# Kernel optimization log

Measured on AMD Instinct MI355X. Metric: run time of the kernel, lower is better.

Reference implementation:

```python
import jax, jax.numpy as jnp
import numpy as np

V = 50000      # vocab_size
E = 300        # EMBED_SIZE
H = 128        # HIDDEN_SIZE // NUM_DIRS
T = 12         # num_tags
SOS = 3
EOS = 4
NEG = -10000.0


def setup_inputs() -> dict:
    key = jax.random.key(0)
    ks = jax.random.split(key, 14)
    B, S = 128, 512
    x = jax.random.randint(ks[0], (B, S), 0, V)
    y0 = jax.random.randint(ks[1], (B, S), 0, T)
    s = 1.0 / np.sqrt(H)
    u = lambda k, shape: jax.random.uniform(k, shape, jnp.float32, -s, s)
    embed = jax.random.normal(ks[2], (V, E), jnp.float32)
    # torch LSTM gate layout: [i, f, g, o] stacked along first dim (4H)
    Wih_f = u(ks[3], (4 * H, E)); Whh_f = u(ks[4], (4 * H, H)); b_f = u(ks[5], (4 * H,)) + u(ks[6], (4 * H,))
    Wih_b = u(ks[7], (4 * H, E)); Whh_b = u(ks[8], (4 * H, H)); b_b = u(ks[9], (4 * H,)) + u(ks[10], (4 * H,))
    Wout = u(ks[11], (T, 2 * H)); bout = u(ks[12], (T,))
    trans = jax.random.normal(ks[13], (T, T), jnp.float32)
    trans = trans.at[SOS, :].set(NEG).at[:, EOS].set(NEG)
    return dict(x=x, y0=y0, embed=embed,
                Wih_f=Wih_f, Whh_f=Whh_f, b_f=b_f,
                Wih_b=Wih_b, Whh_b=Whh_b, b_b=b_b,
                Wout=Wout, bout=bout, trans=trans)


def _lstm_dir(emb, Wih, Whh, b):
    # emb: [B, S, E] -> hidden states [B, S, H] for one direction
    B = emb.shape[0]
    def step(carry, x_t):
        h, c = carry
        g = x_t @ Wih.T + h @ Whh.T + b  # [B, 4H]
        i, f, gg, o = jnp.split(g, 4, axis=-1)
        c = jax.nn.sigmoid(f) * c + jax.nn.sigmoid(i) * jnp.tanh(gg)
        h = jax.nn.sigmoid(o) * jnp.tanh(c)
        return (h, c), h
    init = (jnp.zeros((B, H), emb.dtype), jnp.zeros((B, H), emb.dtype))
    _, hs = jax.lax.scan(step, init, jnp.swapaxes(emb, 0, 1))  # hs: [S, B, H]
    return jnp.swapaxes(hs, 0, 1)


def reference(x, y0, embed, Wih_f, Whh_f, b_f, Wih_b, Whh_b, b_b, Wout, bout, trans):
    # ---- lstm: embed -> biLSTM -> linear, emissions y: [B, S, T]
    emb = embed[x]
    hf = _lstm_dir(emb, Wih_f, Whh_f, b_f)
    hb = _lstm_dir(emb[:, ::-1], Wih_b, Whh_b, b_b)[:, ::-1]
    y = jnp.concatenate([hf, hb], axis=-1) @ Wout.T + bout

    B = x.shape[0]
    # ---- CRF partition Z via forward algorithm (trans[i, j] = score j -> i)
    score0 = jnp.full((B, T), NEG, y.dtype).at[:, SOS].set(0.0)
    def step(score, emit_t):
        new = jax.nn.logsumexp(score[:, None, :] + trans[None, :, :], axis=-1) + emit_t
        return new, None
    scoreZ, _ = jax.lax.scan(step, score0, jnp.swapaxes(y, 0, 1))
    Z = jax.nn.logsumexp(scoreZ + trans[EOS][None, :], axis=-1)  # [B]

    # ---- gold path score (vectorized version of crf.score)
    y0p = jnp.concatenate([jnp.full((B, 1), SOS, y0.dtype), y0], axis=1)  # [B, S+1]
    emit = jnp.take_along_axis(y, y0p[:, 1:, None], axis=2)[..., 0].sum(axis=1)
    tr = trans[y0p[:, 1:], y0p[:, :-1]].sum(axis=1)
    gold = emit + tr + trans[EOS, y0p[:, -1]]

    return Z - gold  # [B] negative log-likelihood per example
```

## Files before the change

kernel.cpp:

```cpp
#include <hip/hip_runtime.h>

typedef unsigned short u16;
typedef __attribute__((ext_vector_type(8))) short short8;
typedef __attribute__((ext_vector_type(4))) float floatx4;

#define SOS 3
#define EOS 4
#define NEGV -10000.0f
#define LOG2E 1.442695041f
#define TWOLOG2E 2.885390082f

__device__ __forceinline__ u16 f2bf(float f) {
  union { float f; unsigned int i; } v; v.f = f;
  unsigned int r = (v.i + 0x7FFFu + ((v.i >> 16) & 1u)) >> 16;
  return (u16)r;
}
__device__ __forceinline__ void gload_lds16(const u16* g, u16* l) {
  __builtin_amdgcn_global_load_lds((const __attribute__((address_space(1))) void*)g,
                                   (__attribute__((address_space(3))) void*)l, 16, 0, 0);
}

__global__ __launch_bounds__(256) void gather_kernel(const float* __restrict__ embed,
                                                     const int* __restrict__ x,
                                                     u16* __restrict__ A) {
  int idx = blockIdx.x * 256 + threadIdx.x;
  int row = idx / 40;
  int c8 = idx - row * 40;
  int col0 = c8 * 8;
  int b = row & 127, t = row >> 7;
  const float* src = embed + (size_t)x[b * 512 + t] * 300 + col0;
  short8 o;
  if (col0 + 8 <= 300) {
    float4 f0 = *(const float4*)(src);
    float4 f1 = *(const float4*)(src + 4);
    o[0] = (short)f2bf(f0.x); o[1] = (short)f2bf(f0.y);
    o[2] = (short)f2bf(f0.z); o[3] = (short)f2bf(f0.w);
    o[4] = (short)f2bf(f1.x); o[5] = (short)f2bf(f1.y);
    o[6] = (short)f2bf(f1.z); o[7] = (short)f2bf(f1.w);
  } else {
    #pragma unroll
    for (int e = 0; e < 8; ++e)
      o[e] = (col0 + e < 300) ? (short)f2bf(src[e]) : (short)0;
  }
  *(short8*)&A[(size_t)row * 320 + col0] = o;
}

__global__ __launch_bounds__(256) void wpack_kernel(const float* __restrict__ Wf,
                                                    const float* __restrict__ Wb,
                                                    u16* __restrict__ Wp) {
  int idx = blockIdx.x * 256 + threadIdx.x;
  int p = idx / 40;
  int c8 = idx - p * 40;
  int col0 = c8 * 8;
  int dd = p >> 9, q = p & 511;
  int j = q >> 2, g = q & 3;
  const float* src = (dd ? Wb : Wf) + (size_t)(g * 128 + j) * 300;
  short8 o;
  #pragma unroll
  for (int e = 0; e < 8; ++e)
    o[e] = (col0 + e < 300) ? (short)f2bf(src[col0 + e]) : (short)0;
  *(short8*)&Wp[(size_t)p * 320 + col0] = o;
}

__global__ __launch_bounds__(256) void gemm_kernel(const u16* __restrict__ A,
                                                   const u16* __restrict__ B,
                                                   const float* __restrict__ bf_,
                                                   const float* __restrict__ bb_,
                                                   u16* __restrict__ G) {
  __shared__ u16 At[128 * 32];
  __shared__ u16 Bt[128 * 32];
  const int n = blockIdx.x;
  const int xcd = n & 7, rr = n >> 3;
  const int bx = xcd * 64 + (rr >> 3);
  const int by = rr & 7;
  const int tid = threadIdx.x;
  const int lane = tid & 63;
  const int wave = tid >> 6;
  const int wr = wave >> 1, wc = wave & 1;
  const int arow0 = bx * 128;
  const int bcol0 = by * 128;
  floatx4 acc[4][4] = {};
  const int fq = lane >> 4;
  const int fr = lane & 15;
  const int sr = wave * 32 + (lane >> 2);
  const int sc = (lane & 3) * 8;
  for (int k0 = 0; k0 < 320; k0 += 32) {
    #pragma unroll
    for (int q = 0; q < 2; ++q) {
      gload_lds16(&A[(size_t)(arow0 + sr + q * 16) * 320 + k0 + sc], &At[wave * 1024 + q * 512]);
      gload_lds16(&B[(size_t)(bcol0 + sr + q * 16) * 320 + k0 + sc], &Bt[wave * 1024 + q * 512]);
    }
    __syncthreads();
    short8 af[4], bfr[4];
    #pragma unroll
    for (int mi = 0; mi < 4; ++mi)
      af[mi] = *(const short8*)&At[(wr * 64 + mi * 16 + fr) * 32 + fq * 8];
    #pragma unroll
    for (int ni = 0; ni < 4; ++ni)
      bfr[ni] = *(const short8*)&Bt[(wc * 64 + ni * 16 + fr) * 32 + fq * 8];
    #pragma unroll
    for (int mi = 0; mi < 4; ++mi)
      #pragma unroll
      for (int ni = 0; ni < 4; ++ni)
        acc[mi][ni] = __builtin_amdgcn_mfma_f32_16x16x32_bf16(af[mi], bfr[ni], acc[mi][ni], 0, 0, 0);
    __syncthreads();
  }
  float biasv[4];
  #pragma unroll
  for (int ni = 0; ni < 4; ++ni) {
    int col = bcol0 + wc * 64 + ni * 16 + fr;
    int dd = col >> 9, q = col & 511;
    int jj = q >> 2, gg = q & 3;
    biasv[ni] = (dd ? bb_ : bf_)[gg * 128 + jj];
  }
  #pragma unroll
  for (int mi = 0; mi < 4; ++mi)
    #pragma unroll
    for (int ni = 0; ni < 4; ++ni)
      #pragma unroll
      for (int r = 0; r < 4; ++r) {
        int row = arow0 + wr * 64 + mi * 16 + fq * 4 + r;
        int col = bcol0 + wc * 64 + ni * 16 + fr;
        G[(size_t)row * 1024 + col] = f2bf(acc[mi][ni][r] + biasv[ni]);
      }
}

__global__ __launch_bounds__(512, 2) void lstm_fused_kernel(const u16* __restrict__ Gp,
                                                            const float* __restrict__ Whh_f,
                                                            const float* __restrict__ Whh_b,
                                                            u16* __restrict__ hs) {
  const int bid = blockIdx.x;
  const int d  = bid >> 5;
  const int b0 = (bid & 31) * 4;
  const int tid = threadIdx.x;
  const int w = tid >> 6, lane = tid & 63;
  const int fr = lane & 15, fq = lane >> 4;
  const float* Wd = d ? Whh_b : Whh_f;

  short8 Wfr[4][4];
  #pragma unroll
  for (int tt = 0; tt < 4; ++tt) {
    const int orow = (fr & 3) * 128 + (16 * w + 4 * tt + (fr >> 2));
    #pragma unroll
    for (int kk = 0; kk < 4; ++kk) {
      const float* src = Wd + (size_t)orow * 128 + fq * 8 + kk * 32;
      float4 x0 = *(const float4*)src;
      float4 x1 = *(const float4*)(src + 4);
      short8 o;
      o[0] = (short)f2bf(x0.x); o[1] = (short)f2bf(x0.y);
      o[2] = (short)f2bf(x0.z); o[3] = (short)f2bf(x0.w);
      o[4] = (short)f2bf(x1.x); o[5] = (short)f2bf(x1.y);
      o[6] = (short)f2bf(x1.z); o[7] = (short)f2bf(x1.w);
      Wfr[tt][kk] = o;
    }
  }

  __shared__ __align__(16) u16 hbuf[2][512];
  for (int i = tid; i < 1024; i += 512) (&hbuf[0][0])[i] = 0;
  __syncthreads();

  const int ts = d ? -1 : 1;
  const int t0 = d ? 511 : 0;
  const int bb  = fr & 3;
  const int ttl = fr >> 2;
  const int jj  = 16 * w + 4 * ttl + fq;

  const int ho0 = bb * 128 + (((fq      + 4 * bb) & 15) << 3);
  const int ho1 = bb * 128 + (((fq + 4  + 4 * bb) & 15) << 3);
  const int ho2 = bb * 128 + (((fq + 8  + 4 * bb) & 15) << 3);
  const int ho3 = bb * 128 + (((fq + 12 + 4 * bb) & 15) << 3);
  const int hwi = bb * 128 + ((((jj >> 3) + 4 * bb) & 15) << 3) + (jj & 7);

  const long long gstep = (long long)ts * 131072;
  const long long hstep = (long long)ts * 256;
  const u16* gld = Gp + (long long)t0 * 131072 + (b0 + bb) * 1024 + d * 512 + 4 * jj;
  u16* hsp = hs + (size_t)(b0 + bb) * 131072 + (long long)t0 * 256 + d * 128 + jj;
  float cst = 0.f;

  uint2 gA, gB, gC;
  gA = *(const uint2*)gld; gld += gstep;
  gB = *(const uint2*)gld; gld += gstep;
  gC = *(const uint2*)gld; gld += gstep;

  u16* hr = &hbuf[0][0];
  u16* hw = &hbuf[1][0];

#define STEPN(GR_, PF_) { \
    short8 f0 = *(const short8*)(hr + ho0); \
    short8 f1 = *(const short8*)(hr + ho1); \
    short8 f2 = *(const short8*)(hr + ho2); \
    short8 f3 = *(const short8*)(hr + ho3); \
    floatx4 a0 = {0.f, 0.f, 0.f, 0.f}; \
    floatx4 a1 = a0, a2 = a0, a3 = a0; \
    a0 = __builtin_amdgcn_mfma_f32_16x16x32_bf16(Wfr[0][0], f0, a0, 0, 0, 0); \
    a1 = __builtin_amdgcn_mfma_f32_16x16x32_bf16(Wfr[1][0], f0, a1, 0, 0, 0); \
    a2 = __builtin_amdgcn_mfma_f32_16x16x32_bf16(Wfr[2][0], f0, a2, 0, 0, 0); \
    a3 = __builtin_amdgcn_mfma_f32_16x16x32_bf16(Wfr[3][0], f0, a3, 0, 0, 0); \
    a0 = __builtin_amdgcn_mfma_f32_16x16x32_bf16(Wfr[0][1], f1, a0, 0, 0, 0); \
    a1 = __builtin_amdgcn_mfma_f32_16x16x32_bf16(Wfr[1][1], f1, a1, 0, 0, 0); \
    a2 = __builtin_amdgcn_mfma_f32_16x16x32_bf16(Wfr[2][1], f1, a2, 0, 0, 0); \
    a3 = __builtin_amdgcn_mfma_f32_16x16x32_bf16(Wfr[3][1], f1, a3, 0, 0, 0); \
    a0 = __builtin_amdgcn_mfma_f32_16x16x32_bf16(Wfr[0][2], f2, a0, 0, 0, 0); \
    a1 = __builtin_amdgcn_mfma_f32_16x16x32_bf16(Wfr[1][2], f2, a1, 0, 0, 0); \
    a2 = __builtin_amdgcn_mfma_f32_16x16x32_bf16(Wfr[2][2], f2, a2, 0, 0, 0); \
    a3 = __builtin_amdgcn_mfma_f32_16x16x32_bf16(Wfr[3][2], f2, a3, 0, 0, 0); \
    a0 = __builtin_amdgcn_mfma_f32_16x16x32_bf16(Wfr[0][3], f3, a0, 0, 0, 0); \
    a1 = __builtin_amdgcn_mfma_f32_16x16x32_bf16(Wfr[1][3], f3, a1, 0, 0, 0); \
    a2 = __builtin_amdgcn_mfma_f32_16x16x32_bf16(Wfr[2][3], f3, a2, 0, 0, 0); \
    a3 = __builtin_amdgcn_mfma_f32_16x16x32_bf16(Wfr[3][3], f3, a3, 0, 0, 0); \
    const bool s0 = (ttl & 1), s1 = (ttl & 2); \
    float p0 = s1 ? (s0 ? a3[0] : a2[0]) : (s0 ? a1[0] : a0[0]); \
    float p1 = s1 ? (s0 ? a3[1] : a2[1]) : (s0 ? a1[1] : a0[1]); \
    float p2 = s1 ? (s0 ? a3[2] : a2[2]) : (s0 ? a1[2] : a0[2]); \
    float p3 = s1 ? (s0 ? a3[3] : a2[3]) : (s0 ? a1[3] : a0[3]); \
    float G0 = __builtin_bit_cast(float, GR_.x << 16); \
    float G1 = __builtin_bit_cast(float, GR_.x & 0xffff0000u); \
    float G2 = __builtin_bit_cast(float, GR_.y << 16); \
    float G3 = __builtin_bit_cast(float, GR_.y & 0xffff0000u); \
    if (PF_) { GR_ = *(const uint2*)gld; gld += gstep; } \
    float i_ = p0 + G0, f_ = p1 + G1, g_ = p2 + G2, o_ = p3 + G3; \
    float p  = __builtin_amdgcn_exp2f(__builtin_amdgcn_fmed3f(g_ * TWOLOG2E, -40.f, 40.f)); \
    float qi = __builtin_amdgcn_exp2f(__builtin_amdgcn_fmed3f(i_ * -LOG2E, -40.f, 40.f)); \
    float qf = __builtin_amdgcn_exp2f(__builtin_amdgcn_fmed3f(f_ * -LOG2E, -40.f, 40.f)); \
    float qo = __builtin_amdgcn_exp2f(__builtin_amdgcn_fmed3f(o_ * -LOG2E, -40.f, 40.f)); \
    float D1 = (1.f + qi) * (p + 1.f); \
    float qf1 = 1.f + qf; \
    float cn = (cst * D1 + (p - 1.f) * qf1) * __builtin_amdgcn_rcpf(qf1 * D1); \
    cst = cn; \
    float v = __builtin_amdgcn_exp2f(__builtin_amdgcn_fmed3f(cn * TWOLOG2E, -40.f, 40.f)); \
    float h = (v - 1.f) * __builtin_amdgcn_rcpf((1.f + qo) * (v + 1.f)); \
    u16 hb = f2bf(h); \
    hw[hwi] = hb; \
    *hsp = hb; \
    hsp += hstep; \
    __builtin_amdgcn_sched_barrier(0); \
    asm volatile("s_waitcnt lgkmcnt(0)"); \
    __builtin_amdgcn_sched_barrier(0); \
    __builtin_amdgcn_s_barrier(); \
    __builtin_amdgcn_sched_barrier(0); \
    u16* tp_ = hr; hr = hw; hw = tp_; \
  }

  #pragma unroll 1
  for (int it = 0; it < 170; ++it) {
    STEPN(gA, true);
    STEPN(gB, true);
    STEPN(gC, true);
  }
  STEPN(gA, false);
  STEPN(gB, false);
#undef STEPN
}

__global__ __launch_bounds__(256) void emis_kernel(const u16* __restrict__ hs,
                                                   const float* __restrict__ Wout,
                                                   const float* __restrict__ bout,
                                                   float* __restrict__ y) {
  __shared__ float Ws[12 * 256];
  __shared__ float bs[12];
  const int tid = threadIdx.x;
  for (int i = tid; i < 12 * 256; i += 256) Ws[i] = Wout[i];
  if (tid < 12) bs[tid] = bout[tid];
  __syncthreads();
  const int wave = tid >> 6, lane = tid & 63;
  const size_t m = (size_t)blockIdx.x * 4 + wave;
  uint2 hv = *(const uint2*)&hs[m * 256 + lane * 4];
  float h0 = __builtin_bit_cast(float, hv.x << 16);
  float h1 = __builtin_bit_cast(float, hv.x & 0xffff0000u);
  float h2 = __builtin_bit_cast(float, hv.y << 16);
  float h3 = __builtin_bit_cast(float, hv.y & 0xffff0000u);
  float p[12];
  #pragma unroll
  for (int tg = 0; tg < 12; ++tg) {
    const float* wv = &Ws[tg * 256 + lane * 4];
    p[tg] = h0 * wv[0] + h1 * wv[1] + h2 * wv[2] + h3 * wv[3];
  }
  #pragma unroll
  for (int off = 32; off; off >>= 1)
    #pragma unroll
    for (int tg = 0; tg < 12; ++tg)
      p[tg] += __shfl_xor(p[tg], off);
  if (lane == 0) {
    #pragma unroll
    for (int tg = 0; tg < 12; ++tg)
      y[m * 12 + tg] = p[tg] + bs[tg];
  }
}

__global__ __launch_bounds__(64) void crf_kernel(const float* __restrict__ y,
                                                 const int* __restrict__ y0,
                                                 const float* __restrict__ trans,
                                                 float* __restrict__ out) {
  const int b = blockIdx.x;
  const int lane = threadIdx.x;
  __shared__ float trs[144];
  for (int i = lane; i < 144; i += 64) trs[i] = trans[i];
  __syncthreads();
  const int row = (lane < 12) ? lane : 0;
  float etr[12];
  #pragma unroll
  for (int j = 0; j < 12; ++j) etr[j] = __expf(trs[row * 12 + j]);
  float etreos = (lane < 12) ? __expf(trs[EOS * 12 + lane]) : 0.f;
  float u = (lane == SOS) ? 1.f : 0.f;
  float base = 0.f;
  const float* yb = y + (size_t)b * 512 * 12;
  float pe0 = __expf(yb[row]);
  float pe1 = __expf(yb[12 + row]);
  for (int t = 0; t < 512; ++t) {
    float pe = pe0;
    pe0 = pe1;
    if (t + 2 < 512) pe1 = __expf(yb[(t + 2) * 12 + row]);
    float U[12];
    #pragma unroll
    for (int j = 0; j < 12; ++j)
      U[j] = __builtin_bit_cast(float, __builtin_amdgcn_readlane(__builtin_bit_cast(int, u), j));
    float m_[12];
    #pragma unroll
    for (int j = 0; j < 12; ++j) m_[j] = etr[j] * U[j];
    float d = (((m_[0] + m_[1]) + (m_[2] + m_[3])) + ((m_[4] + m_[5]) + (m_[6] + m_[7])))
            + ((m_[8] + m_[9]) + (m_[10] + m_[11]));
    float uraw = d * pe;
    float r = __builtin_bit_cast(float, __builtin_amdgcn_readlane(__builtin_bit_cast(int, uraw), 0));
    base += __logf(r);
    u = uraw * __builtin_amdgcn_rcpf(r);
  }
  float vv = (lane < 12) ? u * etreos : 0.f;
  #pragma unroll
  for (int off = 32; off; off >>= 1) vv += __shfl_xor(vv, off);
  const float Z = base + __logf(vv);
  const int* y0b = y0 + (size_t)b * 512;
  float acc = 0.f;
  for (int t = lane; t < 512; t += 64) {
    int cur = y0b[t];
    int prev = t ? y0b[t - 1] : SOS;
    acc += yb[t * 12 + cur] + trs[cur * 12 + prev];
  }
  #pragma unroll
  for (int off = 32; off; off >>= 1) acc += __shfl_xor(acc, off);
  if (lane == 0) {
    float gold = acc + trs[EOS * 12 + y0b[511]];
    out[b] = Z - gold;
  }
}

extern "C" void kernel_launch(void* const* d_in, const int* in_sizes, int n_in,
                              void* d_out, int out_size, void* d_ws, size_t ws_size,
                              hipStream_t stream) {
  (void)in_sizes; (void)n_in; (void)out_size; (void)ws_size;
  const int*   x     = (const int*)d_in[0];
  const int*   y0    = (const int*)d_in[1];
  const float* embed = (const float*)d_in[2];
  const float* Wih_f = (const float*)d_in[3];
  const float* Whh_f = (const float*)d_in[4];
  const float* b_f   = (const float*)d_in[5];
  const float* Wih_b = (const float*)d_in[6];
  const float* Whh_b = (const float*)d_in[7];
  const float* b_b   = (const float*)d_in[8];
  const float* Wout  = (const float*)d_in[9];
  const float* bout  = (const float*)d_in[10];
  const float* trans = (const float*)d_in[11];
  float* out = (float*)d_out;

  char* ws = (char*)d_ws;
  u16*   A  = (u16*)(ws);
  u16*   Wp = (u16*)(ws + 41943040);
  u16*   G  = (u16*)(ws + 42598400);
  u16*   hs = (u16*)(ws + 176816128);
  float* yy = (float*)(ws + 210370560);

  gather_kernel<<<10240, 256, 0, stream>>>(embed, x, A);
  wpack_kernel<<<160, 256, 0, stream>>>(Wih_f, Wih_b, Wp);
  gemm_kernel<<<4096, 256, 0, stream>>>(A, Wp, b_f, b_b, G);
  lstm_fused_kernel<<<64, 512, 0, stream>>>(G, Whh_f, Whh_b, hs);
  emis_kernel<<<16384, 256, 0, stream>>>(hs, Wout, bout, yy);
  crf_kernel<<<128, 64, 0, stream>>>(yy, y0, trans, out);
}
```

Before: 541.2 us.

## Double-buffer GEMM LDS tiles and vectorize transposed epilogue stores

Switches the input-projection GEMM to double-buffered LDS, so the global-to-LDS load of the next K-slice is issued before the MFMAs on the current one, and only one barrier is needed per iteration. The MFMA operands are swapped so each lane's four accumulator entries sit along consecutive output columns. That lets the epilogue write four packed bf16 values as one 8-byte store instead of scalar 2-byte stores. Doubling LDS use per block may reduce occupancy, and the overall effect is limited because the LSTM recurrence likely dominates total time.

```diff
diff --git a/kernel.cpp b/kernel.cpp
--- a/kernel.cpp
+++ b/kernel.cpp
@@ -67,8 +67,8 @@
                                                    const float* __restrict__ bf_,
                                                    const float* __restrict__ bb_,
                                                    u16* __restrict__ G) {
-  __shared__ u16 At[128 * 32];
-  __shared__ u16 Bt[128 * 32];
+  __shared__ u16 At[2][128 * 32];
+  __shared__ u16 Bt[2][128 * 32];
   const int n = blockIdx.x;
   const int xcd = n & 7, rr = n >> 3;
   const int bx = xcd * 64 + (rr >> 3);
@@ -84,45 +84,65 @@
   const int fr = lane & 15;
   const int sr = wave * 32 + (lane >> 2);
   const int sc = (lane & 3) * 8;
-  for (int k0 = 0; k0 < 320; k0 += 32) {
-    #pragma unroll
-    for (int q = 0; q < 2; ++q) {
-      gload_lds16(&A[(size_t)(arow0 + sr + q * 16) * 320 + k0 + sc], &At[wave * 1024 + q * 512]);
-      gload_lds16(&B[(size_t)(bcol0 + sr + q * 16) * 320 + k0 + sc], &Bt[wave * 1024 + q * 512]);
-    }
-    __syncthreads();
+
+#define STAGE(BUF_, K0_) { \
+    gload_lds16(&A[(size_t)(arow0 + sr) * 320 + (K0_) + sc],      &At[BUF_][wave * 1024]); \
+    gload_lds16(&A[(size_t)(arow0 + sr + 16) * 320 + (K0_) + sc], &At[BUF_][wave * 1024 + 512]); \
+    gload_lds16(&B[(size_t)(bcol0 + sr) * 320 + (K0_) + sc],      &Bt[BUF_][wave * 1024]); \
+    gload_lds16(&B[(size_t)(bcol0 + sr + 16) * 320 + (K0_) + sc], &Bt[BUF_][wave * 1024 + 512]); \
+  }
+
+  STAGE(0, 0);
+  __builtin_amdgcn_sched_barrier(0);
+  asm volatile("s_waitcnt vmcnt(0)" ::: "memory");
+  __builtin_amdgcn_sched_barrier(0);
+  __builtin_amdgcn_s_barrier();
+  __builtin_amdgcn_sched_barrier(0);
+
+  int cur = 0;
+  #pragma unroll 1
+  for (int ks = 0; ks < 10; ++ks) {
+    if (ks < 9) STAGE(cur ^ 1, (ks + 1) * 32);
     short8 af[4], bfr[4];
     #pragma unroll
     for (int mi = 0; mi < 4; ++mi)
-      af[mi] = *(const short8*)&At[(wr * 64 + mi * 16 + fr) * 32 + fq * 8];
+      af[mi] = *(const short8*)&At[cur][(wr * 64 + mi * 16 + fr) * 32 + fq * 8];
     #pragma unroll
     for (int ni = 0; ni < 4; ++ni)
-      bfr[ni] = *(const short8*)&Bt[(wc * 64 + ni * 16 + fr) * 32 + fq * 8];
+      bfr[ni] = *(const short8*)&Bt[cur][(wc * 64 + ni * 16 + fr) * 32 + fq * 8];
     #pragma unroll
     for (int mi = 0; mi < 4; ++mi)
       #pragma unroll
       for (int ni = 0; ni < 4; ++ni)
-        acc[mi][ni] = __builtin_amdgcn_mfma_f32_16x16x32_bf16(af[mi], bfr[ni], acc[mi][ni], 0, 0, 0);
-    __syncthreads();
-  }
-  float biasv[4];
+        acc[mi][ni] = __builtin_amdgcn_mfma_f32_16x16x32_bf16(bfr[ni], af[mi], acc[mi][ni], 0, 0, 0);
+    __builtin_amdgcn_sched_barrier(0);
+    asm volatile("s_waitcnt vmcnt(0)" ::: "memory");
+    __builtin_amdgcn_sched_barrier(0);
+    __builtin_amdgcn_s_barrier();
+    __builtin_amdgcn_sched_barrier(0);
+    cur ^= 1;
+  }
+#undef STAGE
+
   #pragma unroll
   for (int ni = 0; ni < 4; ++ni) {
-    int col = bcol0 + wc * 64 + ni * 16 + fr;
-    int dd = col >> 9, q = col & 511;
-    int jj = q >> 2, gg = q & 3;
-    biasv[ni] = (dd ? bb_ : bf_)[gg * 128 + jj];
-  }
-  #pragma unroll
-  for (int mi = 0; mi < 4; ++mi)
-    #pragma unroll
-    for (int ni = 0; ni < 4; ++ni)
-      #pragma unroll
-      for (int r = 0; r < 4; ++r) {
-        int row = arow0 + wr * 64 + mi * 16 + fq * 4 + r;
-        int col = bcol0 + wc * 64 + ni * 16 + fr;
-        G[(size_t)row * 1024 + col] = f2bf(acc[mi][ni][r] + biasv[ni]);
-      }
+    const int colq = bcol0 + wc * 64 + ni * 16 + fq * 4;
+    const int jj = (colq & 511) >> 2;
+    const float* bsrc = (colq >= 512) ? bb_ : bf_;
+    const float b0 = bsrc[jj], b1 = bsrc[128 + jj], b2 = bsrc[256 + jj], b3 = bsrc[384 + jj];
+    #pragma unroll
+    for (int mi = 0; mi < 4; ++mi) {
+      const int row = arow0 + wr * 64 + mi * 16 + fr;
+      unsigned q0 = f2bf(acc[mi][ni][0] + b0);
+      unsigned q1 = f2bf(acc[mi][ni][1] + b1);
+      unsigned q2 = f2bf(acc[mi][ni][2] + b2);
+      unsigned q3 = f2bf(acc[mi][ni][3] + b3);
+      uint2 pk;
+      pk.x = q0 | (q1 << 16);
+      pk.y = q2 | (q3 << 16);
+      *(uint2*)&G[(size_t)row * 1024 + colq] = pk;
+    }
+  }
 }
 
 __global__ __launch_bounds__(512, 2) void lstm_fused_kernel(const u16* __restrict__ Gp,
```

New measurement: 555.9 us. +2.7%, slower.
